# Kernel tuning notes

Hardware: AMD Instinct MI355X
Metric: run time of the kernel (lower is better)

The kernel has to match this reference:

```python
import jax, jax.numpy as jnp
import numpy as np

B = 16384
LATENT = 16
HID = 512
STYLE = 64
D = 10  # num_domains


def setup_inputs() -> dict:
    key = jax.random.key(0)
    ks = jax.random.split(key, 20)
    s = 0.02
    inp = {
        "z": jax.random.normal(ks[0], (B, LATENT), jnp.float32),
        "y": jax.random.randint(ks[1], (B,), 0, D, jnp.int32),
        "W0": jax.random.normal(ks[2], (LATENT, HID), jnp.float32) * s,
        "b0": jnp.zeros((HID,), jnp.float32),
        "W1": jax.random.normal(ks[3], (HID, HID), jnp.float32) * s,
        "b1": jnp.zeros((HID,), jnp.float32),
        "W2": jax.random.normal(ks[4], (HID, HID), jnp.float32) * s,
        "b2": jnp.zeros((HID,), jnp.float32),
        "W3": jax.random.normal(ks[5], (HID, HID), jnp.float32) * s,
        "b3": jnp.zeros((HID,), jnp.float32),
        "Wu1": jax.random.normal(ks[6], (D, HID, HID), jnp.float32) * s,
        "bu1": jnp.zeros((D, HID), jnp.float32),
        "Wu2": jax.random.normal(ks[7], (D, HID, HID), jnp.float32) * s,
        "bu2": jnp.zeros((D, HID), jnp.float32),
        "Wu3": jax.random.normal(ks[8], (D, HID, HID), jnp.float32) * s,
        "bu3": jnp.zeros((D, HID), jnp.float32),
        "Wo": jax.random.normal(ks[9], (D, HID, STYLE), jnp.float32) * s,
        "bo": jnp.zeros((D, STYLE), jnp.float32),
    }
    return inp


def reference(z, y, W0, b0, W1, b1, W2, b2, W3, b3,
              Wu1, bu1, Wu2, bu2, Wu3, bu3, Wo, bo):
    # shared trunk
    h = jax.nn.relu(z @ W0 + b0)
    h = jax.nn.relu(h @ W1 + b1)
    h = jax.nn.relu(h @ W2 + b2)
    h = jax.nn.relu(h @ W3 + b3)            # [B, HID]
    # all unshared heads computed densely (as in the original torch.stack)
    t = jax.nn.relu(jnp.einsum('bh,dhk->bdk', h, Wu1) + bu1)   # [B, D, HID]
    t = jax.nn.relu(jnp.einsum('bdh,dhk->bdk', t, Wu2) + bu2)
    t = jax.nn.relu(jnp.einsum('bdh,dhk->bdk', t, Wu3) + bu3)
    out = jnp.einsum('bdh,dhk->bdk', t, Wo) + bo               # [B, D, STYLE]
    # gather the branch indexed by y for each sample
    s = out[jnp.arange(z.shape[0]), y]                          # [B, STYLE]
    return s
```

## Files before the change

kernel.cpp:

```cpp
#include <hip/hip_runtime.h>

#define NB 16384
#define NDOM 10
#define HIDN 512
#define STYLE 64
#define NWIN 512

typedef short bf16x8 __attribute__((ext_vector_type(8)));
typedef float f32x16 __attribute__((ext_vector_type(16)));

#define MFMA __builtin_amdgcn_mfma_f32_32x32x16_bf16


__device__ __forceinline__ unsigned bfr_hi(float x) {
    unsigned u = __float_as_uint(x);
    return (u + 0x7fffu + ((u >> 16) & 1u)) & 0xffff0000u;
}

__device__ __forceinline__ unsigned cvtpk(float a, float b) {
    unsigned r;
    asm("v_cvt_pk_bf16_f32 %0, %1, %2" : "=v"(r) : "v"(a), "v"(b));
    return r;
}

__device__ __forceinline__ void cvhalf2(const float4& x, const float4& y, uint4& h, uint4& l) {
    float xs[8] = {x.x, x.y, x.z, x.w, y.x, y.y, y.z, y.w};
    unsigned hh[8], ll[8];
#pragma unroll
    for (int i = 0; i < 8; ++i) {
        unsigned hb = bfr_hi(xs[i]);
        hh[i] = hb;
        ll[i] = bfr_hi(xs[i] - __uint_as_float(hb));
    }
    h = make_uint4((hh[0] >> 16) | (hh[1] & 0xffff0000u), (hh[2] >> 16) | (hh[3] & 0xffff0000u),
                   (hh[4] >> 16) | (hh[5] & 0xffff0000u), (hh[6] >> 16) | (hh[7] & 0xffff0000u));
    l = make_uint4((ll[0] >> 16) | (ll[1] & 0xffff0000u), (ll[2] >> 16) | (ll[3] & 0xffff0000u),
                   (ll[4] >> 16) | (ll[5] & 0xffff0000u), (ll[6] >> 16) | (ll[7] & 0xffff0000u));
}


__global__ void k_scatter(const int* __restrict__ y, const int* __restrict__ counts,
                          int* __restrict__ cursors, int* __restrict__ rowidx) {
    __shared__ int soff[NDOM];
    if (threadIdx.x == 0) {
        int s = 0;
        for (int dd = 0; dd < NDOM; ++dd) { soff[dd] = s; s += counts[dd]; }
    }
    __syncthreads();
    int b = blockIdx.x * 256 + threadIdx.x;
    int d = y[b];
    int lane = threadIdx.x & 63;
#pragma unroll
    for (int dd = 0; dd < NDOM; ++dd) {
        unsigned long long bal = __ballot(d == dd);
        if (bal == 0ULL) continue;
        int leader = __builtin_ctzll(bal);
        int base = 0;
        if (d == dd && lane == leader)
            base = atomicAdd(&cursors[dd], (int)__popcll(bal));
        base = __shfl(base, leader);
        if (d == dd) {
            int rank = (int)__popcll(bal & ((1ULL << lane) - 1ULL));
            rowidx[soff[dd] + base + rank] = b;
        }
    }
}


__global__ void k_prep(const float* __restrict__ W1, const float* __restrict__ W2,
                       const float* __restrict__ W3, const float* __restrict__ Wu1,
                       const float* __restrict__ Wu2, const float* __restrict__ Wu3,
                       const float* __restrict__ W0, const float* __restrict__ Wo,
                       const int* __restrict__ y,
                       short* __restrict__ Wp, short* __restrict__ W0p,
                       short* __restrict__ WoP, int* __restrict__ counts)
{
    const int b = blockIdx.x;
    const int t = threadIdx.x;
    if (b < 2112) {
        __shared__ float Ld[64][66];
        const int mat = b >> 6, wq = (b >> 3) & 7, s = b & 7;
        const float* src;
        if (mat < 3) src = (mat == 0 ? W1 : (mat == 1 ? W2 : W3));
        else {
            int g = (mat - 3) / 10, d = (mat - 3) % 10;
            src = (g == 0 ? Wu1 : (g == 1 ? Wu2 : Wu3)) + (size_t)d * HIDN * HIDN;
        }
        short* dst = Wp + (size_t)mat * 262144 + wq * 32768;
        const int r4 = t >> 6, c = t & 63;
#pragma unroll
        for (int p = 0; p < 16; ++p) {
            int k = s * 64 + p * 4 + r4;
            Ld[p * 4 + r4][c] = src[(size_t)k * HIDN + wq * 64 + c];
        }
        __syncthreads();
#pragma unroll
        for (int i = 0; i < 2; ++i) {
            int g = i * 256 + t;
            int ksl = g >> 7, of = (g >> 6) & 1, k8 = (g >> 5) & 1, c5 = g & 31;
            int kk = ksl * 16 + k8 * 8;
            unsigned pk[4];
#pragma unroll
            for (int j2 = 0; j2 < 4; ++j2) {
                unsigned h0 = bfr_hi(Ld[kk + 2 * j2][of * 32 + c5]);
                unsigned h1 = bfr_hi(Ld[kk + 2 * j2 + 1][of * 32 + c5]);
                pk[j2] = (h0 >> 16) | (h1 & 0xffff0000u);
            }
            int ksg = s * 4 + ksl;
            *(uint4*)(dst + ksg * 1024 + of * 512 + k8 * 256 + c5 * 8) =
                make_uint4(pk[0], pk[1], pk[2], pk[3]);
        }
    } else if (b == 2112) {
#pragma unroll
        for (int i = 0; i < 4; ++i) {
            int g = i * 256 + t;
            int wq = g >> 7, of = (g >> 6) & 1, k8 = (g >> 5) & 1, c5 = g & 31;
            int col = wq * 64 + of * 32 + c5;
            unsigned pk[4];
#pragma unroll
            for (int j2 = 0; j2 < 4; ++j2) {
                unsigned h0 = bfr_hi(W0[(size_t)(k8 * 8 + 2 * j2) * HIDN + col]);
                unsigned h1 = bfr_hi(W0[(size_t)(k8 * 8 + 2 * j2 + 1) * HIDN + col]);
                pk[j2] = (h0 >> 16) | (h1 & 0xffff0000u);
            }
            *(uint4*)(W0p + g * 8) = make_uint4(pk[0], pk[1], pk[2], pk[3]);
        }
    } else if (b < 2123) {
        const int dom = b - 2113;
        const float* src = Wo + (size_t)dom * HIDN * STYLE;
        short* dst = WoP + (size_t)dom * 32768;
#pragma unroll
        for (int i = 0; i < 16; ++i) {
            int g = i * 256 + t;
            int w1 = g >> 11, ks = (g >> 6) & 31, k8 = (g >> 5) & 1, c5 = g & 31;
            int col = w1 * 32 + c5;
            int k0 = ks * 16 + k8 * 8;
            unsigned pk[4];
#pragma unroll
            for (int j2 = 0; j2 < 4; ++j2) {
                unsigned h0 = bfr_hi(src[(size_t)(k0 + 2 * j2) * STYLE + col]);
                unsigned h1 = bfr_hi(src[(size_t)(k0 + 2 * j2 + 1) * STYLE + col]);
                pk[j2] = (h0 >> 16) | (h1 & 0xffff0000u);
            }
            *(uint4*)(dst + g * 8) = make_uint4(pk[0], pk[1], pk[2], pk[3]);
        }
    } else {
        int idx = (b - 2123) * 256 + t;
        int d = y[idx];
        int lane = t & 63;
#pragma unroll
        for (int dd = 0; dd < NDOM; ++dd) {
            unsigned long long bal = __ballot(d == dd);
            if (bal != 0ULL && d == dd && lane == __builtin_ctzll(bal))
                atomicAdd(&counts[dd], (int)__popcll(bal));
        }
    }
}


__device__ __forceinline__ void pass512(const short* __restrict__ sH,
                                        const short* __restrict__ pW,
                                        int w, int lane, f32x16& acc)
{
#pragma unroll
    for (int e = 0; e < 16; ++e) acc[e] = 0.f;
    const int rb = (lane & 31) * 8;
    const int lh = lane >> 5;
    const short* p = pW + (w >> 1) * 32768 + (w & 1) * 512 + lane * 8;
    bf16x8 wv[4];
#pragma unroll
    for (int d = 0; d < 4; ++d) wv[d] = *(const bf16x8*)(p + d * 1024);
    bf16x8 hb[2];
    hb[0] = *(const bf16x8*)(sH + lh * 256 + rb);
#pragma unroll
    for (int ks = 0; ks < 32; ++ks) {
        const int pc = ks & 1, pn = pc ^ 1;
        bf16x8 wk = wv[ks & 3];
        if (ks < 28) wv[ks & 3] = *(const bf16x8*)(p + (ks + 4) * 1024);
        if (ks < 31)
            hb[pn] = *(const bf16x8*)(sH + (2 * (ks + 1) + lh) * 256 + rb);
        acc = MFMA(wk, hb[pc], acc, 0, 0, 0);
    }
}

template<bool RELU>
__device__ __forceinline__ void epi512(short* __restrict__ sH, f32x16& acc,
                                       const float* __restrict__ bias,
                                       int w, int lane, int rlo, int rhi)
{
    const int lh = lane >> 5;
    const int row = lane & 31;
    const bool pred = (row >= rlo && row < rhi);
    unsigned mh[4][2];
#pragma unroll
    for (int q = 0; q < 4; ++q) {
        const float4 bv = *(const float4*)&bias[w * 32 + q * 8 + lh * 4];
        float v[4];
#pragma unroll
        for (int j = 0; j < 4; ++j) {
            float x = acc[q * 4 + j] + (&bv.x)[j];
            if (RELU) x = fmaxf(x, 0.f);
            v[j] = x;
        }
        mh[q][0] = cvtpk(v[0], v[1]);
        mh[q][1] = cvtpk(v[2], v[3]);
    }
#pragma unroll
    for (int t = 0; t < 2; ++t) {
        const int q = 2 * t + lh;
        const int qs = 2 * t + (lh ^ 1);
        unsigned r0 = (unsigned)__shfl_xor((int)mh[qs][0], 32);
        unsigned r1 = (unsigned)__shfl_xor((int)mh[qs][1], 32);
        uint4 line = lh == 0 ? make_uint4(mh[q][0], mh[q][1], r0, r1)
                             : make_uint4(r0, r1, mh[q][0], mh[q][1]);
        if (pred) *(uint4*)(sH + (w * 4 + q) * 256 + row * 8) = line;
    }
}

__global__ __launch_bounds__(1024, 8)
void k_fused(const float* __restrict__ z, const int* __restrict__ rowidx,
             const int* __restrict__ counts,
             const short* __restrict__ Wp, const short* __restrict__ W0p,
             const short* __restrict__ WoP,
             const float* __restrict__ b0, const float* __restrict__ b1,
             const float* __restrict__ b2, const float* __restrict__ b3,
             const float* __restrict__ bu1, const float* __restrict__ bu2,
             const float* __restrict__ bu3, const float* __restrict__ bo,
             float* __restrict__ out)
{
    __shared__ short sH[16384];
    __shared__ int soff[NDOM + 1];

    const int win = (blockIdx.x & 7) * 64 + (blockIdx.x >> 3);
    const int row0 = win * 32;
    const int tid = threadIdx.x;
    const int lane = tid & 63;
    const int w = tid >> 6;
    const int lh = lane >> 5;

    if (tid == 0) {
        int s = 0;
#pragma unroll
        for (int dd = 0; dd < NDOM; ++dd) { soff[dd] = s; s += counts[dd]; }
        soff[NDOM] = s;
    }

    f32x16 acc;

    {
#pragma unroll
        for (int e = 0; e < 16; ++e) acc[e] = 0.f;
        bf16x8 w0v = *(const bf16x8*)(W0p + (w >> 1) * 1024 + (w & 1) * 512 + lane * 8);
        const int r = lane & 31;
        const int src = rowidx[row0 + r];
        const float* zp = z + (size_t)src * 16 + lh * 8;
        float4 f0 = *(const float4*)zp;
        float4 f1 = *(const float4*)(zp + 4);
        uint4 h, l;
        cvhalf2(f0, f1, h, l);
        bf16x8 zh = *(bf16x8*)&h;
        bf16x8 zl = *(bf16x8*)&l;
        acc = MFMA(w0v, zh, acc, 0, 0, 0);
        acc = MFMA(w0v, zl, acc, 0, 0, 0);
        epi512<true>(sH, acc, b0, w, lane, 0, 32);
        __syncthreads();
    }

#pragma unroll 1
    for (int m = 0; m < 3; ++m) {
        const float* bp = (m == 0) ? b1 : (m == 1) ? b2 : b3;
        pass512(sH, Wp + (size_t)m * 262144, w, lane, acc);
        __syncthreads();
        epi512<true>(sH, acc, bp, w, lane, 0, 32);
        __syncthreads();
    }

#pragma unroll 1
    for (int L = 0; L < 3; ++L) {
        const short* WL_ = Wp + (size_t)(3 + L * 10) * 262144;
        const float* bL = (L == 0) ? bu1 : (L == 1) ? bu2 : bu3;
#pragma unroll 1
        for (int d = 0; d < NDOM; ++d) {
            int rlo = soff[d] - row0, rhi = soff[d + 1] - row0;
            rlo = rlo < 0 ? 0 : rlo;
            rhi = rhi > 32 ? 32 : rhi;
            if (rhi <= rlo) continue;
            pass512(sH, WL_ + (size_t)d * 262144, w, lane, acc);
            __syncthreads();
            epi512<true>(sH, acc, bL + d * HIDN, w, lane, rlo, rhi);
            __syncthreads();
        }
    }

    if (w < 2) {
        const int r = lane & 31;
#pragma unroll 1
        for (int d = 0; d < NDOM; ++d) {
            int rlo = soff[d] - row0, rhi = soff[d + 1] - row0;
            rlo = rlo < 0 ? 0 : rlo;
            rhi = rhi > 32 ? 32 : rhi;
            if (rhi <= rlo) continue;
#pragma unroll
            for (int e = 0; e < 16; ++e) acc[e] = 0.f;
            const short* pw = WoP + (size_t)d * 32768 + w * 16384 + lane * 8;
            bf16x8 wb[4];
#pragma unroll
            for (int dd = 0; dd < 4; ++dd) wb[dd] = *(const bf16x8*)(pw + dd * 512);
#pragma unroll
            for (int ks = 0; ks < 32; ++ks) {
                bf16x8 wk = wb[ks & 3];
                if (ks < 28) wb[ks & 3] = *(const bf16x8*)(pw + (ks + 4) * 512);
                bf16x8 bhv = *(const bf16x8*)(sH + (2 * ks + lh) * 256 + (lane & 31) * 8);
                acc = MFMA(wk, bhv, acc, 0, 0, 0);
            }
            if (r >= rlo && r < rhi) {
                const int orow = rowidx[row0 + r];
                float* op = out + (size_t)orow * STYLE + w * 32 + lh * 4;
                const float* bop = bo + d * STYLE + w * 32 + lh * 4;
#pragma unroll
                for (int q = 0; q < 4; ++q) {
                    float4 v;
                    v.x = acc[q * 4 + 0] + bop[q * 8 + 0];
                    v.y = acc[q * 4 + 1] + bop[q * 8 + 1];
                    v.z = acc[q * 4 + 2] + bop[q * 8 + 2];
                    v.w = acc[q * 4 + 3] + bop[q * 8 + 3];
                    *(float4*)(op + q * 8) = v;
                }
            }
        }
    }
}


extern "C" void kernel_launch(void* const* d_in, const int* in_sizes, int n_in,
                              void* d_out, int out_size, void* d_ws, size_t ws_size,
                              hipStream_t stream) {
    const float* z   = (const float*)d_in[0];
    const int*   y   = (const int*)d_in[1];
    const float* W0  = (const float*)d_in[2];
    const float* b0  = (const float*)d_in[3];
    const float* W1  = (const float*)d_in[4];
    const float* b1  = (const float*)d_in[5];
    const float* W2  = (const float*)d_in[6];
    const float* b2  = (const float*)d_in[7];
    const float* W3  = (const float*)d_in[8];
    const float* b3  = (const float*)d_in[9];
    const float* Wu1 = (const float*)d_in[10];
    const float* bu1 = (const float*)d_in[11];
    const float* Wu2 = (const float*)d_in[12];
    const float* bu2 = (const float*)d_in[13];
    const float* Wu3 = (const float*)d_in[14];
    const float* bu3 = (const float*)d_in[15];
    const float* Wo  = (const float*)d_in[16];
    const float* bo  = (const float*)d_in[17];
    float* out = (float*)d_out;

    short* Wp   = (short*)d_ws;
    short* W0p  = Wp + (size_t)33 * 262144;
    short* WoP  = W0p + 8192;
    int* rowidx  = (int*)(WoP + (size_t)10 * 32768);
    int* counts  = rowidx + NB;
    int* cursors = counts + NDOM;

    hipMemsetAsync(counts, 0, sizeof(int) * 2 * NDOM, stream);
    k_prep<<<2187, 256, 0, stream>>>(W1, W2, W3, Wu1, Wu2, Wu3, W0, Wo, y,
                                     Wp, W0p, WoP, counts);
    k_scatter<<<NB / 256, 256, 0, stream>>>(y, counts, cursors, rowidx);
    k_fused<<<NWIN, 1024, 0, stream>>>(z, rowidx, counts, Wp, W0p, WoP,
                                       b0, b1, b2, b3, bu1, bu2, bu3, bo, out);
}
```

Measured before the change: 170.7 us.

## Process 64-row windows per block to reuse each weight fragment twice

Each fused block now handles 64 rows instead of 32, with two MFMA accumulators per wave sharing every weight fragment loaded from global memory. This halves weight traffic per row and doubles the shared activation buffer, with domain heads running only the 32-row halves that contain the domain. The prep kernel also loads weights into its transpose tile with float4 reads and a wider padded row. In exchange there are half as many blocks, lower occupancy (launch bounds 4 instead of 8), more registers, and the output stage uses 4 waves.

```diff
diff --git a/kernel.cpp b/kernel.cpp
--- a/kernel.cpp
+++ b/kernel.cpp
@@ -4,7 +4,7 @@
 #define NDOM 10
 #define HIDN 512
 #define STYLE 64
-#define NWIN 512
+#define NWIN 256
 
 typedef short bf16x8 __attribute__((ext_vector_type(8)));
 typedef float f32x16 __attribute__((ext_vector_type(16)));
@@ -78,7 +78,7 @@
     const int b = blockIdx.x;
     const int t = threadIdx.x;
     if (b < 2112) {
-        __shared__ float Ld[64][66];
+        __shared__ float Ld[64][68];
         const int mat = b >> 6, wq = (b >> 3) & 7, s = b & 7;
         const float* src;
         if (mat < 3) src = (mat == 0 ? W1 : (mat == 1 ? W2 : W3));
@@ -87,11 +87,12 @@
             src = (g == 0 ? Wu1 : (g == 1 ? Wu2 : Wu3)) + (size_t)d * HIDN * HIDN;
         }
         short* dst = Wp + (size_t)mat * 262144 + wq * 32768;
-        const int r4 = t >> 6, c = t & 63;
-#pragma unroll
-        for (int p = 0; p < 16; ++p) {
-            int k = s * 64 + p * 4 + r4;
-            Ld[p * 4 + r4][c] = src[(size_t)k * HIDN + wq * 64 + c];
+#pragma unroll
+        for (int i = 0; i < 4; ++i) {
+            int idx = i * 256 + t;
+            int row = idx >> 4, c4 = idx & 15;
+            *(float4*)&Ld[row][c4 * 4] =
+                *(const float4*)(src + (size_t)(s * 64 + row) * HIDN + wq * 64 + c4 * 4);
         }
         __syncthreads();
 #pragma unroll
@@ -158,66 +159,83 @@
 }
 
 
+template<int NFM>
 __device__ __forceinline__ void pass512(const short* __restrict__ sH,
                                         const short* __restrict__ pW,
-                                        int w, int lane, f32x16& acc)
+                                        int w, int lane, f32x16 acc[2])
 {
 #pragma unroll
-    for (int e = 0; e < 16; ++e) acc[e] = 0.f;
+    for (int nf = 0; nf < 2; ++nf)
+        if (NFM & (1 << nf))
+#pragma unroll
+            for (int e = 0; e < 16; ++e) acc[nf][e] = 0.f;
     const int rb = (lane & 31) * 8;
     const int lh = lane >> 5;
     const short* p = pW + (w >> 1) * 32768 + (w & 1) * 512 + lane * 8;
     bf16x8 wv[4];
 #pragma unroll
     for (int d = 0; d < 4; ++d) wv[d] = *(const bf16x8*)(p + d * 1024);
-    bf16x8 hb[2];
-    hb[0] = *(const bf16x8*)(sH + lh * 256 + rb);
+    bf16x8 hb[2][2];
+    const int base0 = lh * 512 + rb;
+#pragma unroll
+    for (int nf = 0; nf < 2; ++nf)
+        if (NFM & (1 << nf)) hb[0][nf] = *(const bf16x8*)(sH + base0 + nf * 256);
 #pragma unroll
     for (int ks = 0; ks < 32; ++ks) {
         const int pc = ks & 1, pn = pc ^ 1;
         bf16x8 wk = wv[ks & 3];
         if (ks < 28) wv[ks & 3] = *(const bf16x8*)(p + (ks + 4) * 1024);
-        if (ks < 31)
-            hb[pn] = *(const bf16x8*)(sH + (2 * (ks + 1) + lh) * 256 + rb);
-        acc = MFMA(wk, hb[pc], acc, 0, 0, 0);
-    }
-}
-
-template<bool RELU>
-__device__ __forceinline__ void epi512(short* __restrict__ sH, f32x16& acc,
+        if (ks < 31) {
+            const int basen = (2 * (ks + 1) + lh) * 512 + rb;
+#pragma unroll
+            for (int nf = 0; nf < 2; ++nf)
+                if (NFM & (1 << nf)) hb[pn][nf] = *(const bf16x8*)(sH + basen + nf * 256);
+        }
+#pragma unroll
+        for (int nf = 0; nf < 2; ++nf)
+            if (NFM & (1 << nf)) acc[nf] = MFMA(wk, hb[pc][nf], acc[nf], 0, 0, 0);
+    }
+}
+
+template<int NFM, bool RELU>
+__device__ __forceinline__ void epi512(short* __restrict__ sH, f32x16 acc[2],
                                        const float* __restrict__ bias,
                                        int w, int lane, int rlo, int rhi)
 {
     const int lh = lane >> 5;
-    const int row = lane & 31;
-    const bool pred = (row >= rlo && row < rhi);
-    unsigned mh[4][2];
-#pragma unroll
-    for (int q = 0; q < 4; ++q) {
-        const float4 bv = *(const float4*)&bias[w * 32 + q * 8 + lh * 4];
-        float v[4];
-#pragma unroll
-        for (int j = 0; j < 4; ++j) {
-            float x = acc[q * 4 + j] + (&bv.x)[j];
-            if (RELU) x = fmaxf(x, 0.f);
-            v[j] = x;
-        }
-        mh[q][0] = cvtpk(v[0], v[1]);
-        mh[q][1] = cvtpk(v[2], v[3]);
-    }
-#pragma unroll
-    for (int t = 0; t < 2; ++t) {
-        const int q = 2 * t + lh;
-        const int qs = 2 * t + (lh ^ 1);
-        unsigned r0 = (unsigned)__shfl_xor((int)mh[qs][0], 32);
-        unsigned r1 = (unsigned)__shfl_xor((int)mh[qs][1], 32);
-        uint4 line = lh == 0 ? make_uint4(mh[q][0], mh[q][1], r0, r1)
-                             : make_uint4(r0, r1, mh[q][0], mh[q][1]);
-        if (pred) *(uint4*)(sH + (w * 4 + q) * 256 + row * 8) = line;
-    }
-}
-
-__global__ __launch_bounds__(1024, 8)
+#pragma unroll
+    for (int nf = 0; nf < 2; ++nf) {
+        if (!(NFM & (1 << nf))) continue;
+        const int row = nf * 32 + (lane & 31);
+        const bool pred = (row >= rlo && row < rhi);
+        unsigned mh[4][2];
+#pragma unroll
+        for (int q = 0; q < 4; ++q) {
+            const float4 bv = *(const float4*)&bias[w * 32 + q * 8 + lh * 4];
+            float v[4];
+#pragma unroll
+            for (int j = 0; j < 4; ++j) {
+                float x = acc[nf][q * 4 + j] + (&bv.x)[j];
+                if (RELU) x = fmaxf(x, 0.f);
+                v[j] = x;
+            }
+            mh[q][0] = cvtpk(v[0], v[1]);
+            mh[q][1] = cvtpk(v[2], v[3]);
+        }
+#pragma unroll
+        for (int t = 0; t < 2; ++t) {
+            const int q = 2 * t + lh;
+            const int qs = 2 * t + (lh ^ 1);
+            unsigned r0 = (unsigned)__shfl_xor((int)mh[qs][0], 32);
+            unsigned r1 = (unsigned)__shfl_xor((int)mh[qs][1], 32);
+            uint4 line = lh == 0 ? make_uint4(mh[q][0], mh[q][1], r0, r1)
+                                 : make_uint4(r0, r1, mh[q][0], mh[q][1]);
+            if (pred) *(uint4*)(sH + (w * 4 + q) * 512 + row * 8) = line;
+        }
+    }
+}
+
+__global__ __launch_bounds__(1024, 4)
 void k_fused(const float* __restrict__ z, const int* __restrict__ rowidx,
              const int* __restrict__ counts,
              const short* __restrict__ Wp, const short* __restrict__ W0p,
@@ -228,11 +246,11 @@
              const float* __restrict__ bu3, const float* __restrict__ bo,
              float* __restrict__ out)
 {
-    __shared__ short sH[16384];
+    __shared__ short sH[32768];
     __shared__ int soff[NDOM + 1];
 
-    const int win = (blockIdx.x & 7) * 64 + (blockIdx.x >> 3);
-    const int row0 = win * 32;
+    const int win = (blockIdx.x & 7) * 32 + (blockIdx.x >> 3);
+    const int row0 = win * 64;
     const int tid = threadIdx.x;
     const int lane = tid & 63;
     const int w = tid >> 6;
@@ -245,33 +263,36 @@
         soff[NDOM] = s;
     }
 
-    f32x16 acc;
+    f32x16 acc[2];
 
     {
-#pragma unroll
-        for (int e = 0; e < 16; ++e) acc[e] = 0.f;
         bf16x8 w0v = *(const bf16x8*)(W0p + (w >> 1) * 1024 + (w & 1) * 512 + lane * 8);
-        const int r = lane & 31;
-        const int src = rowidx[row0 + r];
-        const float* zp = z + (size_t)src * 16 + lh * 8;
-        float4 f0 = *(const float4*)zp;
-        float4 f1 = *(const float4*)(zp + 4);
-        uint4 h, l;
-        cvhalf2(f0, f1, h, l);
-        bf16x8 zh = *(bf16x8*)&h;
-        bf16x8 zl = *(bf16x8*)&l;
-        acc = MFMA(w0v, zh, acc, 0, 0, 0);
-        acc = MFMA(w0v, zl, acc, 0, 0, 0);
-        epi512<true>(sH, acc, b0, w, lane, 0, 32);
+#pragma unroll
+        for (int nf = 0; nf < 2; ++nf) {
+#pragma unroll
+            for (int e = 0; e < 16; ++e) acc[nf][e] = 0.f;
+            const int r = nf * 32 + (lane & 31);
+            const int src = rowidx[row0 + r];
+            const float* zp = z + (size_t)src * 16 + lh * 8;
+            float4 f0 = *(const float4*)zp;
+            float4 f1 = *(const float4*)(zp + 4);
+            uint4 h, l;
+            cvhalf2(f0, f1, h, l);
+            bf16x8 zh = *(bf16x8*)&h;
+            bf16x8 zl = *(bf16x8*)&l;
+            acc[nf] = MFMA(w0v, zh, acc[nf], 0, 0, 0);
+            acc[nf] = MFMA(w0v, zl, acc[nf], 0, 0, 0);
+        }
+        epi512<3, true>(sH, acc, b0, w, lane, 0, 64);
         __syncthreads();
     }
 
 #pragma unroll 1
     for (int m = 0; m < 3; ++m) {
         const float* bp = (m == 0) ? b1 : (m == 1) ? b2 : b3;
-        pass512(sH, Wp + (size_t)m * 262144, w, lane, acc);
+        pass512<3>(sH, Wp + (size_t)m * 262144, w, lane, acc);
         __syncthreads();
-        epi512<true>(sH, acc, bp, w, lane, 0, 32);
+        epi512<3, true>(sH, acc, bp, w, lane, 0, 64);
         __syncthreads();
     }
 
@@ -283,47 +304,57 @@
         for (int d = 0; d < NDOM; ++d) {
             int rlo = soff[d] - row0, rhi = soff[d + 1] - row0;
             rlo = rlo < 0 ? 0 : rlo;
-            rhi = rhi > 32 ? 32 : rhi;
+            rhi = rhi > 64 ? 64 : rhi;
             if (rhi <= rlo) continue;
-            pass512(sH, WL_ + (size_t)d * 262144, w, lane, acc);
+            const int nfm = (rlo < 32 ? 1 : 0) | (rhi > 32 ? 2 : 0);
+            const short* pw = WL_ + (size_t)d * 262144;
+            if (nfm == 3)      pass512<3>(sH, pw, w, lane, acc);
+            else if (nfm == 1) pass512<1>(sH, pw, w, lane, acc);
+            else               pass512<2>(sH, pw, w, lane, acc);
             __syncthreads();
-            epi512<true>(sH, acc, bL + d * HIDN, w, lane, rlo, rhi);
+            if (nfm == 3)      epi512<3, true>(sH, acc, bL + d * HIDN, w, lane, rlo, rhi);
+            else if (nfm == 1) epi512<1, true>(sH, acc, bL + d * HIDN, w, lane, rlo, rhi);
+            else               epi512<2, true>(sH, acc, bL + d * HIDN, w, lane, rlo, rhi);
             __syncthreads();
         }
     }
 
-    if (w < 2) {
-        const int r = lane & 31;
+    if (w < 4) {
+        const int rh = w >> 1, ch = w & 1;
+        const int r = rh * 32 + (lane & 31);
 #pragma unroll 1
         for (int d = 0; d < NDOM; ++d) {
             int rlo = soff[d] - row0, rhi = soff[d + 1] - row0;
             rlo = rlo < 0 ? 0 : rlo;
-            rhi = rhi > 32 ? 32 : rhi;
+            rhi = rhi > 64 ? 64 : rhi;
             if (rhi <= rlo) continue;
-#pragma unroll
-            for (int e = 0; e < 16; ++e) acc[e] = 0.f;
-            const short* pw = WoP + (size_t)d * 32768 + w * 16384 + lane * 8;
+            if (rhi <= rh * 32 || rlo >= rh * 32 + 32) continue;
+            f32x16 fa;
+#pragma unroll
+            for (int e = 0; e < 16; ++e) fa[e] = 0.f;
+            const short* pw = WoP + (size_t)d * 32768 + ch * 16384 + lane * 8;
             bf16x8 wb[4];
 #pragma unroll
             for (int dd = 0; dd < 4; ++dd) wb[dd] = *(const bf16x8*)(pw + dd * 512);
+            const int hbase = (rh * 32 + (lane & 31)) * 8;
 #pragma unroll
             for (int ks = 0; ks < 32; ++ks) {
                 bf16x8 wk = wb[ks & 3];
                 if (ks < 28) wb[ks & 3] = *(const bf16x8*)(pw + (ks + 4) * 512);
-                bf16x8 bhv = *(const bf16x8*)(sH + (2 * ks + lh) * 256 + (lane & 31) * 8);
-                acc = MFMA(wk, bhv, acc, 0, 0, 0);
+                bf16x8 bhv = *(const bf16x8*)(sH + (2 * ks + lh) * 512 + hbase);
+                fa = MFMA(wk, bhv, fa, 0, 0, 0);
             }
             if (r >= rlo && r < rhi) {
                 const int orow = rowidx[row0 + r];
-                float* op = out + (size_t)orow * STYLE + w * 32 + lh * 4;
-                const float* bop = bo + d * STYLE + w * 32 + lh * 4;
+                float* op = out + (size_t)orow * STYLE + ch * 32 + lh * 4;
+                const float* bop = bo + d * STYLE + ch * 32 + lh * 4;
 #pragma unroll
                 for (int q = 0; q < 4; ++q) {
                     float4 v;
-                    v.x = acc[q * 4 + 0] + bop[q * 8 + 0];
-                    v.y = acc[q * 4 + 1] + bop[q * 8 + 1];
-                    v.z = acc[q * 4 + 2] + bop[q * 8 + 2];
-                    v.w = acc[q * 4 + 3] + bop[q * 8 + 3];
+                    v.x = fa[q * 4 + 0] + bop[q * 8 + 0];
+                    v.y = fa[q * 4 + 1] + bop[q * 8 + 1];
+                    v.z = fa[q * 4 + 2] + bop[q * 8 + 2];
+                    v.w = fa[q * 4 + 3] + bop[q * 8 + 3];
                     *(float4*)(op + q * 8) = v;
                 }
             }
```

Measured after the change: 162.7 us. 4.7% less time.
